# Kernel tuning notes

Measured on AMD Instinct MI355X. Metric: run time of the kernel, lower is better.

The kernel has to match this reference:

```python
import jax, jax.numpy as jnp
import numpy as np

NUM_GROUPS = 6
K = 40
CODEBOOK = 1024
VQ_COMMIT = 0.25


def setup_inputs() -> dict:
    key = jax.random.key(0)
    k1, k2 = jax.random.split(key)
    z = jax.random.normal(k1, (32, 60, 8000), dtype=jnp.float32)
    embeddings = jax.random.normal(k2, (NUM_GROUPS, K, CODEBOOK), dtype=jnp.float32)
    return {"z": z, "embeddings": embeddings}


def reference(z, embeddings):
    # z: (N, 60, T) -> reshape to (N, 240, T//4) as in Group_Quantize.forward
    N, C, T = z.shape
    z2 = z.reshape(N, C * 4, -1)          # (N, 240, Tp)
    Tp = z2.shape[-1]
    # split into groups and move channel last (EMAQuantizer transposes 1,-1)
    x = z2.reshape(N, NUM_GROUPS, K, Tp)
    x = jnp.transpose(x, (1, 0, 3, 2))    # (G, N, Tp, K)
    flat = x.reshape(NUM_GROUPS, N * Tp, K)  # (G, R, K)

    dist = (jnp.sum(flat ** 2, axis=-1, keepdims=True)
            - 2.0 * jnp.einsum('grk,gkc->grc', flat, embeddings)
            + jnp.sum(embeddings ** 2, axis=1)[:, None, :])  # (G, R, C)
    idx = jnp.argmin(dist, axis=-1)       # (G, R)

    # codebook lookup per group (embedding stored as (K, C), code vectors are columns)
    quant = jax.vmap(lambda e, i: jnp.take(e.T, i, axis=0))(embeddings, idx)  # (G, R, K)

    x4 = x                                 # (G, N, Tp, K)
    q4 = quant.reshape(NUM_GROUPS, N, Tp, K)

    # commitment loss per group, per batch element
    diff = VQ_COMMIT * jnp.mean((jax.lax.stop_gradient(q4) - x4) ** 2, axis=(2, 3))  # (G, N)
    vq_loss = jnp.sum(diff, axis=0) / NUM_GROUPS  # (N,)

    # straight-through estimator
    q_ste = x4 + jax.lax.stop_gradient(q4 - x4)   # (G, N, Tp, K)
    q_merge = jnp.transpose(q_ste, (1, 0, 3, 2)).reshape(N, NUM_GROUPS * K, Tp)  # (N, 240, Tp)
    q_merge = q_merge.reshape(N, (NUM_GROUPS * K) // 4, -1)  # (N, 60, T)
    return q_merge, vq_loss
```

## Files before the change

kernel.cpp:

```cpp
#include <hip/hip_runtime.h>
#include <math.h>

#define NG 6
#define KD 40
#define CB 1024
#define NB 32
#define TP 2000
#define RPB 128
#define THREADS 256
#define NBLK 500
#define ZN 480000
#define ZG 80000
#define BAND_D 6e-3f
#define PK_G 98304
#define PK_T 3072
#define CHS 6144
#define NCH 16

typedef __attribute__((ext_vector_type(8))) short bf16x8;
typedef __attribute__((ext_vector_type(16))) float f32x16;

__device__ __forceinline__ unsigned short bf16rne(float v) {
  unsigned u = __float_as_uint(v);
  return (unsigned short)((u + 0x7FFFu + ((u >> 16) & 1u)) >> 16);
}
__device__ __forceinline__ float bf16val(unsigned short h) {
  return __uint_as_float(((unsigned)h) << 16);
}
__device__ __forceinline__ void bf16split(float v, unsigned short& h, unsigned short& l) {
  h = bf16rne(v);
  l = bf16rne(v - bf16val(h));
}
__device__ __forceinline__ bf16x8 ldfrag16(const unsigned short* p) {
  union { uint4 q; bf16x8 v; } u;
  u.q = *(const uint4*)p;
  return u.v;
}
__device__ __forceinline__ void gload_lds16(const void* g, void* l) {
  __builtin_amdgcn_global_load_lds(
      (const __attribute__((address_space(1))) unsigned int*)g,
      (__attribute__((address_space(3))) unsigned int*)l, 16, 0, 0);
}

__global__ void prep_kernel(const float* __restrict__ emb, float* __restrict__ et,
                            float* __restrict__ e2, unsigned short* __restrict__ epack) {
  int c = blockIdx.x * blockDim.x + threadIdx.x;
  int g = blockIdx.y;
  if (c >= CB) return;
  const float* eg = emb + (size_t)g * KD * CB;
  float ev[KD];
  float* o = et + ((size_t)g * CB + c) * KD;
  float s = 0.f;
#pragma unroll
  for (int k = 0; k < KD; ++k) {
    float v = eg[k * CB + c];
    ev[k] = v;
    o[k] = v;
    s = __fadd_rn(s, __fmul_rn(v, v));
  }
  e2[g * CB + c] = s;

  float sv = 0.5f * s;
  unsigned short p0 = bf16rne(sv);
  float v1 = sv - bf16val(p0);
  unsigned short p1 = bf16rne(v1);
  unsigned short p2 = bf16rne(v1 - bf16val(p1));

  int tile = c >> 5, j32 = c & 31;
  unsigned short* tb = epack + (size_t)g * PK_G + (size_t)tile * PK_T;
#pragma unroll
  for (int s2 = 0; s2 < 3; ++s2)
#pragma unroll
    for (int gg = 0; gg < 2; ++gg) {
      union { uint4 q; unsigned short sh[8]; } uh, ul;
#pragma unroll
      for (int j = 0; j < 8; ++j) {
        int k = s2 * 16 + gg * 8 + j;
        if (k < KD) {
          bf16split(ev[k], uh.sh[j], ul.sh[j]);
        } else {
          uh.sh[j] = (k == 40) ? p0 : (k == 41) ? p1 : (k == 42) ? p2 : (unsigned short)0;
          ul.sh[j] = 0;
        }
      }
      unsigned short* ph = tb + ((size_t)(s2 * 2 + gg) * 32 + j32) * 8;
      *(uint4*)ph = uh.q;
      *(uint4*)(ph + 1536) = ul.q;
    }
}

__device__ __forceinline__ float npd_calc(const float* __restrict__ x,
                                          const float* __restrict__ ef,
                                          float e2c, float x2np) {
  float dot = 0.f;
#pragma unroll
  for (int k = 0; k < KD; ++k) dot = __fadd_rn(dot, __fmul_rn(x[k], ef[k]));
  return __fadd_rn(__fsub_rn(x2np, __fadd_rn(dot, dot)), e2c);
}

__global__ __launch_bounds__(THREADS, 4) void vq_kernel(
    const float* __restrict__ z, const float* __restrict__ et,
    const float* __restrict__ e2, const unsigned short* __restrict__ epack,
    float* __restrict__ out, float* __restrict__ partials) {
  const int g = blockIdx.y;
  const int bb = blockIdx.x;
  const int tid = threadIdx.x;
  const int lane = tid & 63;
  const int gg = lane >> 5;
  const int j32 = lane & 31;
  const int wid = tid >> 6;
  const int rowloc = wid * 32 + j32;
  const int rid = bb * RPB + rowloc;
  const int n = rid / TP;
  const int tt = rid - n * TP;

  const float* etg = et + (size_t)g * CB * KD;
  const float* e2g = e2 + g * CB;
  const unsigned short* egrp = epack + (size_t)g * PK_G;

  __shared__ __align__(16) unsigned short sbuf[2][CHS];
  __shared__ float r0s[THREADS], r1s[THREADS];

#define STAGE(B, CH) { \
    const unsigned short* gsrc = egrp + (size_t)(CH) * CHS + wid * 512 + lane * 8; \
    unsigned short* lb = &sbuf[B][wid * 512]; \
    gload_lds16(gsrc, lb); \
    gload_lds16(gsrc + 2048, lb + 2048); \
    gload_lds16(gsrc + 4096, lb + 4096); }
  STAGE(0, 0)

  const float* zp = z + (size_t)n * ZN + (size_t)g * ZG + tt;
  float x[KD];
#pragma unroll
  for (int k = 0; k < KD; ++k) x[k] = zp[(size_t)k * TP];
  float x2np;
  {
    float r[8];
#pragma unroll
    for (int j = 0; j < 8; ++j) r[j] = __fmul_rn(x[j], x[j]);
#pragma unroll
    for (int i = 8; i < KD; i += 8)
#pragma unroll
      for (int j = 0; j < 8; ++j)
        r[j] = __fadd_rn(r[j], __fmul_rn(x[i + j], x[i + j]));
    x2np = __fadd_rn(__fadd_rn(__fadd_rn(r[0], r[1]), __fadd_rn(r[2], r[3])),
                     __fadd_rn(__fadd_rn(r[4], r[5]), __fadd_rn(r[6], r[7])));
  }

  bf16x8 xh[3], xl[3];
#define PACK8(DH, DL, B0) { \
    union { unsigned short s[8]; bf16x8 v; } uh, ul; \
    _Pragma("unroll") \
    for (int j = 0; j < 8; ++j) { \
      unsigned short h, l; bf16split(-x[(B0) + j], h, l); \
      uh.s[j] = h; ul.s[j] = l; } \
    DH = uh.v; DL = ul.v; }
  if (gg == 0) {
    PACK8(xh[0], xl[0], 0)
    PACK8(xh[1], xl[1], 16)
    PACK8(xh[2], xl[2], 32)
  } else {
    PACK8(xh[0], xl[0], 8)
    PACK8(xh[1], xl[1], 24)
    union { unsigned short s[8]; bf16x8 v; } uh;
#pragma unroll
    for (int j = 0; j < 8; ++j) uh.s[j] = (j < 3) ? (unsigned short)0x3F80 : (unsigned short)0;
    xh[2] = uh.v;
    union { unsigned short s[8]; bf16x8 v; } uz;
#pragma unroll
    for (int j = 0; j < 8; ++j) uz.s[j] = 0;
    xl[2] = uz.v;
  }
#undef PACK8

  f32x16 zacc;
#pragma unroll
  for (int i = 0; i < 16; ++i) zacc[i] = 0.f;

  float d1 = INFINITY, d2x = INFINITY;
  int grp1 = 0;

#define TRACKG(AV, TILE) { \
    int cb = (TILE) * 32 + 4 * gg; \
    float g0 = fminf(fminf(fminf(AV[0], AV[1]), AV[2]), AV[3]); \
    float g1 = fminf(fminf(fminf(AV[4], AV[5]), AV[6]), AV[7]); \
    float g2 = fminf(fminf(fminf(AV[8], AV[9]), AV[10]), AV[11]); \
    float g3 = fminf(fminf(fminf(AV[12], AV[13]), AV[14]), AV[15]); \
    d2x = fminf(d2x, fmaxf(d1, g0)); grp1 = (g0 < d1) ? (cb + 0) : grp1; d1 = fminf(d1, g0); \
    d2x = fminf(d2x, fmaxf(d1, g1)); grp1 = (g1 < d1) ? (cb + 8) : grp1; d1 = fminf(d1, g1); \
    d2x = fminf(d2x, fmaxf(d1, g2)); grp1 = (g2 < d1) ? (cb + 16) : grp1; d1 = fminf(d1, g2); \
    d2x = fminf(d2x, fmaxf(d1, g3)); grp1 = (g3 < d1) ? (cb + 24) : grp1; d1 = fminf(d1, g3); }

#define MFMA9(TB, AOUT) { \
    bf16x8 eh0 = ldfrag16(TB); \
    bf16x8 eh1 = ldfrag16((TB) + 512); \
    bf16x8 eh2 = ldfrag16((TB) + 1024); \
    bf16x8 el0 = ldfrag16((TB) + 1536); \
    bf16x8 el1 = ldfrag16((TB) + 2048); \
    bf16x8 el2 = ldfrag16((TB) + 2560); \
    AOUT = __builtin_amdgcn_mfma_f32_32x32x16_bf16(eh0, xh[0], zacc, 0, 0, 0); \
    AOUT = __builtin_amdgcn_mfma_f32_32x32x16_bf16(eh0, xl[0], AOUT, 0, 0, 0); \
    AOUT = __builtin_amdgcn_mfma_f32_32x32x16_bf16(el0, xh[0], AOUT, 0, 0, 0); \
    AOUT = __builtin_amdgcn_mfma_f32_32x32x16_bf16(eh1, xh[1], AOUT, 0, 0, 0); \
    AOUT = __builtin_amdgcn_mfma_f32_32x32x16_bf16(eh1, xl[1], AOUT, 0, 0, 0); \
    AOUT = __builtin_amdgcn_mfma_f32_32x32x16_bf16(el1, xh[1], AOUT, 0, 0, 0); \
    AOUT = __builtin_amdgcn_mfma_f32_32x32x16_bf16(eh2, xh[2], AOUT, 0, 0, 0); \
    AOUT = __builtin_amdgcn_mfma_f32_32x32x16_bf16(eh2, xl[2], AOUT, 0, 0, 0); \
    AOUT = __builtin_amdgcn_mfma_f32_32x32x16_bf16(el2, xh[2], AOUT, 0, 0, 0); }

  int cur = 0;
#pragma unroll 1
  for (int ch = 0; ch < NCH; ++ch) {
    if (ch + 1 < NCH) {
      STAGE(cur ^ 1, ch + 1)
      asm volatile("s_waitcnt vmcnt(3)" ::: "memory");
    } else {
      asm volatile("s_waitcnt vmcnt(0)" ::: "memory");
    }
    __builtin_amdgcn_s_barrier();
    {
      const unsigned short* tb0 = &sbuf[cur][lane * 8];
      f32x16 a0;
      MFMA9(tb0, a0)
      TRACKG(a0, ch * 2)
      const unsigned short* tb1 = &sbuf[cur][PK_T + lane * 8];
      f32x16 a1;
      MFMA9(tb1, a1)
      TRACKG(a1, ch * 2 + 1)
    }
    __builtin_amdgcn_s_barrier();
    cur ^= 1;
  }

  float bd = INFINITY;
  int bi = CB;
#pragma unroll
  for (int j = 0; j < 4; ++j) {
    int c = grp1 + j;
    float d = npd_calc(x, etg + (size_t)c * KD, e2g[c], x2np);
    if (d < bd) { bd = d; bi = c; }
  }
  float dd2x = fmaf(2.f, d2x, x2np);

  {
    float od = __shfl_xor(bd, 32);
    int oi = __shfl_xor(bi, 32);
    float odd2x = __shfl_xor(dd2x, 32);
    if (od < bd || (od == bd && oi < bi)) { bd = od; bi = oi; }
    dd2x = fminf(dd2x, odd2x);
  }
  bool flag = dd2x < bd + BAND_D;

  if (__any(flag)) {
    float rd1 = INFINITY, rd2 = INFINITY, rd3 = INFINITY;
    int ri1 = 0, ri2 = 0, ri3 = 0;
#define INS3(V, C) { \
      bool u1 = (V) < rd1, u2 = (V) < rd2, u3 = (V) < rd3; \
      rd3 = u2 ? rd2 : (u3 ? (V) : rd3); ri3 = u2 ? ri2 : (u3 ? (C) : ri3); \
      rd2 = u1 ? rd1 : (u2 ? (V) : rd2); ri2 = u1 ? ri1 : (u2 ? (C) : ri2); \
      rd1 = u1 ? (V) : rd1;              ri1 = u1 ? (C) : ri1; }
#pragma unroll 1
    for (int tile = 0; tile < 32; ++tile) {
      const unsigned short* tb = egrp + (size_t)tile * PK_T + lane * 8;
      f32x16 a;
      MFMA9(tb, a)
      {
        float gm0 = fminf(fminf(a[0], a[1]), fminf(a[2], a[3]));
        float gm1 = fminf(fminf(a[4], a[5]), fminf(a[6], a[7]));
        float gm2 = fminf(fminf(a[8], a[9]), fminf(a[10], a[11]));
        float gm3 = fminf(fminf(a[12], a[13]), fminf(a[14], a[15]));
        float tmin = fminf(fminf(gm0, gm1), fminf(gm2, gm3));
        if (tmin < rd3) {
          int cb = tile * 32 + 4 * gg;
          if (gm0 < rd3) { INS3(a[0], cb + 0) INS3(a[1], cb + 1) INS3(a[2], cb + 2) INS3(a[3], cb + 3) }
          if (gm1 < rd3) { INS3(a[4], cb + 8) INS3(a[5], cb + 9) INS3(a[6], cb + 10) INS3(a[7], cb + 11) }
          if (gm2 < rd3) { INS3(a[8], cb + 16) INS3(a[9], cb + 17) INS3(a[10], cb + 18) INS3(a[11], cb + 19) }
          if (gm3 < rd3) { INS3(a[12], cb + 24) INS3(a[13], cb + 25) INS3(a[14], cb + 26) INS3(a[15], cb + 27) }
        }
      }
    }
    float dd1 = fmaf(2.f, rd1, x2np);
    float dd2 = fmaf(2.f, rd2, x2np);
    float dd3 = fmaf(2.f, rd3, x2np);
    bd = dd1; bi = ri1;
    bool exact = false;
    {
      bool need2 = dd2 < dd1 + BAND_D;
      bool need3 = dd3 < dd1 + BAND_D;
      if (need2 || need3) {
        int cA = ri1;
        int cB = need2 ? ri2 : 0x7fffffff;
        int cC = need3 ? ri3 : 0x7fffffff;
        int t;
        if (cA > cB) { t = cA; cA = cB; cB = t; }
        if (cB > cC) { t = cB; cB = cC; cC = t; }
        if (cA > cB) { t = cA; cA = cB; cB = t; }
        bd = INFINITY; bi = CB;
        if (cA < CB) { float d = npd_calc(x, etg + (size_t)cA * KD, e2g[cA], x2np); if (d < bd) { bd = d; bi = cA; } }
        if (cB < CB) { float d = npd_calc(x, etg + (size_t)cB * KD, e2g[cB], x2np); if (d < bd) { bd = d; bi = cB; } }
        if (cC < CB) { float d = npd_calc(x, etg + (size_t)cC * KD, e2g[cC], x2np); if (d < bd) { bd = d; bi = cC; } }
        exact = true;
      }
    }
    {
      float od = __shfl_xor(bd, 32);
      bool race = fabsf(bd - od) < BAND_D;
      if (race && !exact) bd = npd_calc(x, etg + (size_t)bi * KD, e2g[bi], x2np);
      float od2 = __shfl_xor(bd, 32);
      int oi = __shfl_xor(bi, 32);
      if (od2 < bd || (od2 == bd && oi < bi)) { bd = od2; bi = oi; }
    }
  }

  const float4* eb4 = (const float4*)(etg + (size_t)bi * KD);
  float* op = out + (size_t)n * ZN + (size_t)g * ZG + tt;
  float ls = 0.f;
  if (gg == 0) {
#pragma unroll
    for (int p = 0; p < 5; ++p) {
      float4 v = eb4[p];
      int k = 4 * p;
      float e0 = __fsub_rn(v.x, x[k + 0]); ls = fmaf(e0, e0, ls); op[(size_t)(k + 0) * TP] = __fadd_rn(x[k + 0], e0);
      float e1 = __fsub_rn(v.y, x[k + 1]); ls = fmaf(e1, e1, ls); op[(size_t)(k + 1) * TP] = __fadd_rn(x[k + 1], e1);
      float e2v = __fsub_rn(v.z, x[k + 2]); ls = fmaf(e2v, e2v, ls); op[(size_t)(k + 2) * TP] = __fadd_rn(x[k + 2], e2v);
      float e3 = __fsub_rn(v.w, x[k + 3]); ls = fmaf(e3, e3, ls); op[(size_t)(k + 3) * TP] = __fadd_rn(x[k + 3], e3);
    }
  } else {
#pragma unroll
    for (int p = 5; p < 10; ++p) {
      float4 v = eb4[p];
      int k = 4 * p;
      float e0 = __fsub_rn(v.x, x[k + 0]); ls = fmaf(e0, e0, ls); op[(size_t)(k + 0) * TP] = __fadd_rn(x[k + 0], e0);
      float e1 = __fsub_rn(v.y, x[k + 1]); ls = fmaf(e1, e1, ls); op[(size_t)(k + 1) * TP] = __fadd_rn(x[k + 1], e1);
      float e2v = __fsub_rn(v.z, x[k + 2]); ls = fmaf(e2v, e2v, ls); op[(size_t)(k + 2) * TP] = __fadd_rn(x[k + 2], e2v);
      float e3 = __fsub_rn(v.w, x[k + 3]); ls = fmaf(e3, e3, ls); op[(size_t)(k + 3) * TP] = __fadd_rn(x[k + 3], e3);
    }
  }

  const int n_lo = (bb * RPB) / TP;
  r0s[tid] = (n == n_lo) ? ls : 0.f;
  r1s[tid] = (n == n_lo) ? 0.f : ls;
  __syncthreads();
  for (int s = THREADS / 2; s > 0; s >>= 1) {
    if (tid < s) {
      r0s[tid] += r0s[tid + s];
      r1s[tid] += r1s[tid + s];
    }
    __syncthreads();
  }
  if (tid == 0) {
    partials[((size_t)g * NBLK + bb) * 2 + 0] = r0s[0];
    partials[((size_t)g * NBLK + bb) * 2 + 1] = r1s[0];
  }
}

__global__ void loss_kernel(const float* __restrict__ partials,
                            float* __restrict__ vq) {
  int n = threadIdx.x;
  if (n >= NB) return;
  float acc = 0.f;
  for (int g = 0; g < NG; ++g) {
    float s = 0.f;
    int b0 = (n * TP) / RPB;
    int b1 = ((n + 1) * TP - 1) / RPB;
    for (int b = b0; b <= b1; ++b) {
      int n_lo = (b * RPB) / TP;
      s += partials[((size_t)g * NBLK + b) * 2 + ((n == n_lo) ? 0 : 1)];
    }
    acc += 0.25f * (s / 80000.0f);
  }
  vq[n] = acc / 6.0f;
}

extern "C" void kernel_launch(void* const* d_in, const int* in_sizes, int n_in,
                              void* d_out, int out_size, void* d_ws, size_t ws_size,
                              hipStream_t stream) {
  const float* z = (const float*)d_in[0];
  const float* emb = (const float*)d_in[1];
  float* out = (float*)d_out;

  float* et = (float*)d_ws;
  float* e2 = et + (size_t)NG * CB * KD;
  float* partials = e2 + (size_t)NG * CB;
  unsigned short* epack = (unsigned short*)((char*)d_ws + 1031680);

  prep_kernel<<<dim3(CB / 256, NG), 256, 0, stream>>>(emb, et, e2, epack);
  vq_kernel<<<dim3(NBLK, NG), THREADS, 0, stream>>>(z, et, e2, epack, out, partials);
  loss_kernel<<<1, 64, 0, stream>>>(partials, out + (size_t)NB * 60 * 8000);
}
```

Measured before the change: 205.6 us.

## Switch codebook to single fp16 with split-x and widen rescore band

```diff
diff --git a/kernel.cpp b/kernel.cpp
--- a/kernel.cpp
+++ b/kernel.cpp
@@ -11,28 +11,27 @@
 #define NBLK 500
 #define ZN 480000
 #define ZG 80000
-#define BAND_D 6e-3f
-#define PK_G 98304
-#define PK_T 3072
+#define BAND_D 6e-2f
+#define PKH_G 49152
+#define PKH_T 1536
 #define CHS 6144
-#define NCH 16
-
-typedef __attribute__((ext_vector_type(8))) short bf16x8;
+#define NCH 8
+
+typedef __attribute__((ext_vector_type(8))) _Float16 f16x8;
 typedef __attribute__((ext_vector_type(16))) float f32x16;
 
-__device__ __forceinline__ unsigned short bf16rne(float v) {
-  unsigned u = __float_as_uint(v);
-  return (unsigned short)((u + 0x7FFFu + ((u >> 16) & 1u)) >> 16);
-}
-__device__ __forceinline__ float bf16val(unsigned short h) {
-  return __uint_as_float(((unsigned)h) << 16);
-}
-__device__ __forceinline__ void bf16split(float v, unsigned short& h, unsigned short& l) {
-  h = bf16rne(v);
-  l = bf16rne(v - bf16val(h));
-}
-__device__ __forceinline__ bf16x8 ldfrag16(const unsigned short* p) {
-  union { uint4 q; bf16x8 v; } u;
+__device__ __forceinline__ unsigned short f16h(float v) {
+  union { _Float16 h; unsigned short s; } u;
+  u.h = (_Float16)v;
+  return u.s;
+}
+__device__ __forceinline__ float f16f(unsigned short s) {
+  union { _Float16 h; unsigned short s; } u;
+  u.s = s;
+  return (float)u.h;
+}
+__device__ __forceinline__ f16x8 ldfragh(const unsigned short* p) {
+  union { uint4 q; f16x8 v; } u;
   u.q = *(const uint4*)p;
   return u.v;
 }
@@ -43,7 +42,7 @@
 }
 
 __global__ void prep_kernel(const float* __restrict__ emb, float* __restrict__ et,
-                            float* __restrict__ e2, unsigned short* __restrict__ epack) {
+                            float* __restrict__ e2, unsigned short* __restrict__ epackh) {
   int c = blockIdx.x * blockDim.x + threadIdx.x;
   int g = blockIdx.y;
   if (c >= CB) return;
@@ -61,31 +60,23 @@
   e2[g * CB + c] = s;
 
   float sv = 0.5f * s;
-  unsigned short p0 = bf16rne(sv);
-  float v1 = sv - bf16val(p0);
-  unsigned short p1 = bf16rne(v1);
-  unsigned short p2 = bf16rne(v1 - bf16val(p1));
+  unsigned short p0 = f16h(sv);
+  unsigned short p1 = f16h(sv - f16f(p0));
 
   int tile = c >> 5, j32 = c & 31;
-  unsigned short* tb = epack + (size_t)g * PK_G + (size_t)tile * PK_T;
+  unsigned short* tb = epackh + (size_t)g * PKH_G + (size_t)tile * PKH_T;
 #pragma unroll
   for (int s2 = 0; s2 < 3; ++s2)
 #pragma unroll
     for (int gg = 0; gg < 2; ++gg) {
-      union { uint4 q; unsigned short sh[8]; } uh, ul;
+      union { uint4 q; unsigned short sh[8]; } uh;
 #pragma unroll
       for (int j = 0; j < 8; ++j) {
         int k = s2 * 16 + gg * 8 + j;
-        if (k < KD) {
-          bf16split(ev[k], uh.sh[j], ul.sh[j]);
-        } else {
-          uh.sh[j] = (k == 40) ? p0 : (k == 41) ? p1 : (k == 42) ? p2 : (unsigned short)0;
-          ul.sh[j] = 0;
-        }
+        if (k < KD) uh.sh[j] = f16h(ev[k]);
+        else uh.sh[j] = (k == 40) ? p0 : (k == 41) ? p1 : (unsigned short)0;
       }
-      unsigned short* ph = tb + ((size_t)(s2 * 2 + gg) * 32 + j32) * 8;
-      *(uint4*)ph = uh.q;
-      *(uint4*)(ph + 1536) = ul.q;
+      *(uint4*)(tb + ((size_t)(s2 * 2 + gg) * 32 + j32) * 8) = uh.q;
     }
 }
 
@@ -98,9 +89,9 @@
   return __fadd_rn(__fsub_rn(x2np, __fadd_rn(dot, dot)), e2c);
 }
 
-__global__ __launch_bounds__(THREADS, 4) void vq_kernel(
+__global__ __launch_bounds__(THREADS, 3) void vq_kernel(
     const float* __restrict__ z, const float* __restrict__ et,
-    const float* __restrict__ e2, const unsigned short* __restrict__ epack,
+    const float* __restrict__ e2, const unsigned short* __restrict__ epackh,
     float* __restrict__ out, float* __restrict__ partials) {
   const int g = blockIdx.y;
   const int bb = blockIdx.x;
@@ -116,7 +107,7 @@
 
   const float* etg = et + (size_t)g * CB * KD;
   const float* e2g = e2 + g * CB;
-  const unsigned short* egrp = epack + (size_t)g * PK_G;
+  const unsigned short* egrp = epackh + (size_t)g * PKH_G;
 
   __shared__ __align__(16) unsigned short sbuf[2][CHS];
   __shared__ float r0s[THREADS], r1s[THREADS];
@@ -147,31 +138,32 @@
                      __fadd_rn(__fadd_rn(r[4], r[5]), __fadd_rn(r[6], r[7])));
   }
 
-  bf16x8 xh[3], xl[3];
-#define PACK8(DH, DL, B0) { \
-    union { unsigned short s[8]; bf16x8 v; } uh, ul; \
+  f16x8 xh[3], xl[3];
+#define PACKF(DH, DL, B0) { \
+    union { unsigned short s[8]; f16x8 v; } uh, ul; \
     _Pragma("unroll") \
     for (int j = 0; j < 8; ++j) { \
-      unsigned short h, l; bf16split(-x[(B0) + j], h, l); \
-      uh.s[j] = h; ul.s[j] = l; } \
+      float y = -x[(B0) + j]; \
+      unsigned short h = f16h(y); \
+      uh.s[j] = h; ul.s[j] = f16h(y - f16f(h)); } \
     DH = uh.v; DL = ul.v; }
   if (gg == 0) {
-    PACK8(xh[0], xl[0], 0)
-    PACK8(xh[1], xl[1], 16)
-    PACK8(xh[2], xl[2], 32)
+    PACKF(xh[0], xl[0], 0)
+    PACKF(xh[1], xl[1], 16)
+    PACKF(xh[2], xl[2], 32)
   } else {
-    PACK8(xh[0], xl[0], 8)
-    PACK8(xh[1], xl[1], 24)
-    union { unsigned short s[8]; bf16x8 v; } uh;
-#pragma unroll
-    for (int j = 0; j < 8; ++j) uh.s[j] = (j < 3) ? (unsigned short)0x3F80 : (unsigned short)0;
-    xh[2] = uh.v;
-    union { unsigned short s[8]; bf16x8 v; } uz;
-#pragma unroll
-    for (int j = 0; j < 8; ++j) uz.s[j] = 0;
+    PACKF(xh[0], xl[0], 8)
+    PACKF(xh[1], xl[1], 24)
+    union { unsigned short s[8]; f16x8 v; } uo, uz;
+#pragma unroll
+    for (int j = 0; j < 8; ++j) {
+      uo.s[j] = (j < 2) ? (unsigned short)0x3C00 : (unsigned short)0;
+      uz.s[j] = 0;
+    }
+    xh[2] = uo.v;
     xl[2] = uz.v;
   }
-#undef PACK8
+#undef PACKF
 
   f32x16 zacc;
 #pragma unroll
@@ -182,31 +174,25 @@
 
 #define TRACKG(AV, TILE) { \
     int cb = (TILE) * 32 + 4 * gg; \
-    float g0 = fminf(fminf(fminf(AV[0], AV[1]), AV[2]), AV[3]); \
-    float g1 = fminf(fminf(fminf(AV[4], AV[5]), AV[6]), AV[7]); \
-    float g2 = fminf(fminf(fminf(AV[8], AV[9]), AV[10]), AV[11]); \
-    float g3 = fminf(fminf(fminf(AV[12], AV[13]), AV[14]), AV[15]); \
-    d2x = fminf(d2x, fmaxf(d1, g0)); grp1 = (g0 < d1) ? (cb + 0) : grp1; d1 = fminf(d1, g0); \
-    d2x = fminf(d2x, fmaxf(d1, g1)); grp1 = (g1 < d1) ? (cb + 8) : grp1; d1 = fminf(d1, g1); \
-    d2x = fminf(d2x, fmaxf(d1, g2)); grp1 = (g2 < d1) ? (cb + 16) : grp1; d1 = fminf(d1, g2); \
-    d2x = fminf(d2x, fmaxf(d1, g3)); grp1 = (g3 < d1) ? (cb + 24) : grp1; d1 = fminf(d1, g3); }
-
-#define MFMA9(TB, AOUT) { \
-    bf16x8 eh0 = ldfrag16(TB); \
-    bf16x8 eh1 = ldfrag16((TB) + 512); \
-    bf16x8 eh2 = ldfrag16((TB) + 1024); \
-    bf16x8 el0 = ldfrag16((TB) + 1536); \
-    bf16x8 el1 = ldfrag16((TB) + 2048); \
-    bf16x8 el2 = ldfrag16((TB) + 2560); \
-    AOUT = __builtin_amdgcn_mfma_f32_32x32x16_bf16(eh0, xh[0], zacc, 0, 0, 0); \
-    AOUT = __builtin_amdgcn_mfma_f32_32x32x16_bf16(eh0, xl[0], AOUT, 0, 0, 0); \
-    AOUT = __builtin_amdgcn_mfma_f32_32x32x16_bf16(el0, xh[0], AOUT, 0, 0, 0); \
-    AOUT = __builtin_amdgcn_mfma_f32_32x32x16_bf16(eh1, xh[1], AOUT, 0, 0, 0); \
-    AOUT = __builtin_amdgcn_mfma_f32_32x32x16_bf16(eh1, xl[1], AOUT, 0, 0, 0); \
-    AOUT = __builtin_amdgcn_mfma_f32_32x32x16_bf16(el1, xh[1], AOUT, 0, 0, 0); \
-    AOUT = __builtin_amdgcn_mfma_f32_32x32x16_bf16(eh2, xh[2], AOUT, 0, 0, 0); \
-    AOUT = __builtin_amdgcn_mfma_f32_32x32x16_bf16(eh2, xl[2], AOUT, 0, 0, 0); \
-    AOUT = __builtin_amdgcn_mfma_f32_32x32x16_bf16(el2, xh[2], AOUT, 0, 0, 0); }
+    float q0 = fminf(fminf(fminf(AV[0], AV[1]), AV[2]), AV[3]); \
+    float q1 = fminf(fminf(fminf(AV[4], AV[5]), AV[6]), AV[7]); \
+    float q2 = fminf(fminf(fminf(AV[8], AV[9]), AV[10]), AV[11]); \
+    float q3 = fminf(fminf(fminf(AV[12], AV[13]), AV[14]), AV[15]); \
+    d2x = fminf(d2x, fmaxf(d1, q0)); grp1 = (q0 < d1) ? (cb + 0) : grp1; d1 = fminf(d1, q0); \
+    d2x = fminf(d2x, fmaxf(d1, q1)); grp1 = (q1 < d1) ? (cb + 8) : grp1; d1 = fminf(d1, q1); \
+    d2x = fminf(d2x, fmaxf(d1, q2)); grp1 = (q2 < d1) ? (cb + 16) : grp1; d1 = fminf(d1, q2); \
+    d2x = fminf(d2x, fmaxf(d1, q3)); grp1 = (q3 < d1) ? (cb + 24) : grp1; d1 = fminf(d1, q3); }
+
+#define MFMA6(TB, AOUT) { \
+    f16x8 e0 = ldfragh(TB); \
+    f16x8 e1 = ldfragh((TB) + 512); \
+    f16x8 e2f = ldfragh((TB) + 1024); \
+    AOUT = __builtin_amdgcn_mfma_f32_32x32x16_f16(e0, xh[0], zacc, 0, 0, 0); \
+    AOUT = __builtin_amdgcn_mfma_f32_32x32x16_f16(e0, xl[0], AOUT, 0, 0, 0); \
+    AOUT = __builtin_amdgcn_mfma_f32_32x32x16_f16(e1, xh[1], AOUT, 0, 0, 0); \
+    AOUT = __builtin_amdgcn_mfma_f32_32x32x16_f16(e1, xl[1], AOUT, 0, 0, 0); \
+    AOUT = __builtin_amdgcn_mfma_f32_32x32x16_f16(e2f, xh[2], AOUT, 0, 0, 0); \
+    AOUT = __builtin_amdgcn_mfma_f32_32x32x16_f16(e2f, xl[2], AOUT, 0, 0, 0); }
 
   int cur = 0;
 #pragma unroll 1
@@ -219,14 +205,15 @@
     }
     __builtin_amdgcn_s_barrier();
     {
-      const unsigned short* tb0 = &sbuf[cur][lane * 8];
-      f32x16 a0;
-      MFMA9(tb0, a0)
-      TRACKG(a0, ch * 2)
-      const unsigned short* tb1 = &sbuf[cur][PK_T + lane * 8];
-      f32x16 a1;
-      MFMA9(tb1, a1)
-      TRACKG(a1, ch * 2 + 1)
+      f32x16 a0, a1, a2, a3;
+      MFMA6(&sbuf[cur][0 * PKH_T + lane * 8], a0)
+      MFMA6(&sbuf[cur][1 * PKH_T + lane * 8], a1)
+      MFMA6(&sbuf[cur][2 * PKH_T + lane * 8], a2)
+      MFMA6(&sbuf[cur][3 * PKH_T + lane * 8], a3)
+      TRACKG(a0, ch * 4 + 0)
+      TRACKG(a1, ch * 4 + 1)
+      TRACKG(a2, ch * 4 + 2)
+      TRACKG(a3, ch * 4 + 3)
     }
     __builtin_amdgcn_s_barrier();
     cur ^= 1;
@@ -261,9 +248,9 @@
       rd1 = u1 ? (V) : rd1;              ri1 = u1 ? (C) : ri1; }
 #pragma unroll 1
     for (int tile = 0; tile < 32; ++tile) {
-      const unsigned short* tb = egrp + (size_t)tile * PK_T + lane * 8;
+      const unsigned short* tb = egrp + (size_t)tile * PKH_T + lane * 8;
       f32x16 a;
-      MFMA9(tb, a)
+      MFMA6(tb, a)
       {
         float gm0 = fminf(fminf(a[0], a[1]), fminf(a[2], a[3]));
         float gm1 = fminf(fminf(a[4], a[5]), fminf(a[6], a[7]));
@@ -382,9 +369,9 @@
   float* et = (float*)d_ws;
   float* e2 = et + (size_t)NG * CB * KD;
   float* partials = e2 + (size_t)NG * CB;
-  unsigned short* epack = (unsigned short*)((char*)d_ws + 1031680);
-
-  prep_kernel<<<dim3(CB / 256, NG), 256, 0, stream>>>(emb, et, e2, epack);
-  vq_kernel<<<dim3(NBLK, NG), THREADS, 0, stream>>>(z, et, e2, epack, out, partials);
+  unsigned short* epackh = (unsigned short*)((char*)d_ws + 1031680);
+
+  prep_kernel<<<dim3(CB / 256, NG), 256, 0, stream>>>(emb, et, e2, epackh);
+  vq_kernel<<<dim3(NBLK, NG), THREADS, 0, stream>>>(z, et, e2, epackh, out, partials);
   loss_kernel<<<1, 64, 0, stream>>>(partials, out + (size_t)NB * 60 * 8000);
 }
```

Measured after the change: 260.2 us. +26.6%, slower.

## Track top-two candidate groups to shrink exact-rescan fallback frequency

Applied to the files above, without the earlier changes.

```diff
diff --git a/kernel.cpp b/kernel.cpp
--- a/kernel.cpp
+++ b/kernel.cpp
@@ -98,7 +98,7 @@
   return __fadd_rn(__fsub_rn(x2np, __fadd_rn(dot, dot)), e2c);
 }
 
-__global__ __launch_bounds__(THREADS, 4) void vq_kernel(
+__global__ __launch_bounds__(THREADS, 3) void vq_kernel(
     const float* __restrict__ z, const float* __restrict__ et,
     const float* __restrict__ e2, const unsigned short* __restrict__ epack,
     float* __restrict__ out, float* __restrict__ partials) {
@@ -177,19 +177,35 @@
 #pragma unroll
   for (int i = 0; i < 16; ++i) zacc[i] = 0.f;
 
-  float d1 = INFINITY, d2x = INFINITY;
-  int grp1 = 0;
+  float d1 = INFINITY, d2x = INFINITY, d3x = INFINITY;
+  int grp1 = 0, grp2 = 0;
 
 #define TRACKG(AV, TILE) { \
     int cb = (TILE) * 32 + 4 * gg; \
-    float g0 = fminf(fminf(fminf(AV[0], AV[1]), AV[2]), AV[3]); \
-    float g1 = fminf(fminf(fminf(AV[4], AV[5]), AV[6]), AV[7]); \
-    float g2 = fminf(fminf(fminf(AV[8], AV[9]), AV[10]), AV[11]); \
-    float g3 = fminf(fminf(fminf(AV[12], AV[13]), AV[14]), AV[15]); \
-    d2x = fminf(d2x, fmaxf(d1, g0)); grp1 = (g0 < d1) ? (cb + 0) : grp1; d1 = fminf(d1, g0); \
-    d2x = fminf(d2x, fmaxf(d1, g1)); grp1 = (g1 < d1) ? (cb + 8) : grp1; d1 = fminf(d1, g1); \
-    d2x = fminf(d2x, fmaxf(d1, g2)); grp1 = (g2 < d1) ? (cb + 16) : grp1; d1 = fminf(d1, g2); \
-    d2x = fminf(d2x, fmaxf(d1, g3)); grp1 = (g3 < d1) ? (cb + 24) : grp1; d1 = fminf(d1, g3); }
+    float q0 = fminf(fminf(fminf(AV[0], AV[1]), AV[2]), AV[3]); \
+    float q1 = fminf(fminf(fminf(AV[4], AV[5]), AV[6]), AV[7]); \
+    float q2 = fminf(fminf(fminf(AV[8], AV[9]), AV[10]), AV[11]); \
+    float q3 = fminf(fminf(fminf(AV[12], AV[13]), AV[14]), AV[15]); \
+    { bool b1 = q0 < d1, b2 = q0 < d2x; \
+      d3x = fminf(d3x, fmaxf(d2x, q0)); \
+      grp2 = b1 ? grp1 : (b2 ? (cb + 0) : grp2); \
+      d2x = fminf(d2x, fmaxf(d1, q0)); \
+      grp1 = b1 ? (cb + 0) : grp1; d1 = fminf(d1, q0); } \
+    { bool b1 = q1 < d1, b2 = q1 < d2x; \
+      d3x = fminf(d3x, fmaxf(d2x, q1)); \
+      grp2 = b1 ? grp1 : (b2 ? (cb + 8) : grp2); \
+      d2x = fminf(d2x, fmaxf(d1, q1)); \
+      grp1 = b1 ? (cb + 8) : grp1; d1 = fminf(d1, q1); } \
+    { bool b1 = q2 < d1, b2 = q2 < d2x; \
+      d3x = fminf(d3x, fmaxf(d2x, q2)); \
+      grp2 = b1 ? grp1 : (b2 ? (cb + 16) : grp2); \
+      d2x = fminf(d2x, fmaxf(d1, q2)); \
+      grp1 = b1 ? (cb + 16) : grp1; d1 = fminf(d1, q2); } \
+    { bool b1 = q3 < d1, b2 = q3 < d2x; \
+      d3x = fminf(d3x, fmaxf(d2x, q3)); \
+      grp2 = b1 ? grp1 : (b2 ? (cb + 24) : grp2); \
+      d2x = fminf(d2x, fmaxf(d1, q3)); \
+      grp1 = b1 ? (cb + 24) : grp1; d1 = fminf(d1, q3); } }
 
 #define MFMA9(TB, AOUT) { \
     bf16x8 eh0 = ldfrag16(TB); \
@@ -219,13 +235,10 @@
     }
     __builtin_amdgcn_s_barrier();
     {
-      const unsigned short* tb0 = &sbuf[cur][lane * 8];
-      f32x16 a0;
-      MFMA9(tb0, a0)
+      f32x16 a0, a1;
+      MFMA9(&sbuf[cur][lane * 8], a0)
+      MFMA9(&sbuf[cur][PK_T + lane * 8], a1)
       TRACKG(a0, ch * 2)
-      const unsigned short* tb1 = &sbuf[cur][PK_T + lane * 8];
-      f32x16 a1;
-      MFMA9(tb1, a1)
       TRACKG(a1, ch * 2 + 1)
     }
     __builtin_amdgcn_s_barrier();
@@ -234,22 +247,29 @@
 
   float bd = INFINITY;
   int bi = CB;
+#define UPD(DV, CV) { if ((DV) < bd || ((DV) == bd && (CV) < bi)) { bd = (DV); bi = (CV); } }
 #pragma unroll
   for (int j = 0; j < 4; ++j) {
     int c = grp1 + j;
     float d = npd_calc(x, etg + (size_t)c * KD, e2g[c], x2np);
-    if (d < bd) { bd = d; bi = c; }
-  }
-  float dd2x = fmaf(2.f, d2x, x2np);
+    UPD(d, c)
+  }
+#pragma unroll
+  for (int j = 0; j < 4; ++j) {
+    int c = grp2 + j;
+    float d = npd_calc(x, etg + (size_t)c * KD, e2g[c], x2np);
+    UPD(d, c)
+  }
+  float dd3x = fmaf(2.f, d3x, x2np);
 
   {
     float od = __shfl_xor(bd, 32);
     int oi = __shfl_xor(bi, 32);
-    float odd2x = __shfl_xor(dd2x, 32);
+    float odd3x = __shfl_xor(dd3x, 32);
     if (od < bd || (od == bd && oi < bi)) { bd = od; bi = oi; }
-    dd2x = fminf(dd2x, odd2x);
-  }
-  bool flag = dd2x < bd + BAND_D;
+    dd3x = fminf(dd3x, odd3x);
+  }
+  bool flag = dd3x < bd + BAND_D;
 
   if (__any(flag)) {
     float rd1 = INFINITY, rd2 = INFINITY, rd3 = INFINITY;
```

Result: slower. 228.7 us (+11.2%).

## Triple-buffer codebook chunks in LDS and drop the trailing barrier

Applied to the files above, without the earlier changes.

```diff
diff --git a/kernel.cpp b/kernel.cpp
--- a/kernel.cpp
+++ b/kernel.cpp
@@ -98,7 +98,7 @@
   return __fadd_rn(__fsub_rn(x2np, __fadd_rn(dot, dot)), e2c);
 }
 
-__global__ __launch_bounds__(THREADS, 4) void vq_kernel(
+__global__ __launch_bounds__(THREADS, 3) void vq_kernel(
     const float* __restrict__ z, const float* __restrict__ et,
     const float* __restrict__ e2, const unsigned short* __restrict__ epack,
     float* __restrict__ out, float* __restrict__ partials) {
@@ -118,7 +118,7 @@
   const float* e2g = e2 + g * CB;
   const unsigned short* egrp = epack + (size_t)g * PK_G;
 
-  __shared__ __align__(16) unsigned short sbuf[2][CHS];
+  __shared__ __align__(16) unsigned short sbuf[3][CHS];
   __shared__ float r0s[THREADS], r1s[THREADS];
 
 #define STAGE(B, CH) { \
@@ -128,6 +128,7 @@
     gload_lds16(gsrc + 2048, lb + 2048); \
     gload_lds16(gsrc + 4096, lb + 4096); }
   STAGE(0, 0)
+  STAGE(1, 1)
 
   const float* zp = z + (size_t)n * ZN + (size_t)g * ZG + tt;
   float x[KD];
@@ -182,14 +183,14 @@
 
 #define TRACKG(AV, TILE) { \
     int cb = (TILE) * 32 + 4 * gg; \
-    float g0 = fminf(fminf(fminf(AV[0], AV[1]), AV[2]), AV[3]); \
-    float g1 = fminf(fminf(fminf(AV[4], AV[5]), AV[6]), AV[7]); \
-    float g2 = fminf(fminf(fminf(AV[8], AV[9]), AV[10]), AV[11]); \
-    float g3 = fminf(fminf(fminf(AV[12], AV[13]), AV[14]), AV[15]); \
-    d2x = fminf(d2x, fmaxf(d1, g0)); grp1 = (g0 < d1) ? (cb + 0) : grp1; d1 = fminf(d1, g0); \
-    d2x = fminf(d2x, fmaxf(d1, g1)); grp1 = (g1 < d1) ? (cb + 8) : grp1; d1 = fminf(d1, g1); \
-    d2x = fminf(d2x, fmaxf(d1, g2)); grp1 = (g2 < d1) ? (cb + 16) : grp1; d1 = fminf(d1, g2); \
-    d2x = fminf(d2x, fmaxf(d1, g3)); grp1 = (g3 < d1) ? (cb + 24) : grp1; d1 = fminf(d1, g3); }
+    float q0 = fminf(fminf(fminf(AV[0], AV[1]), AV[2]), AV[3]); \
+    float q1 = fminf(fminf(fminf(AV[4], AV[5]), AV[6]), AV[7]); \
+    float q2 = fminf(fminf(fminf(AV[8], AV[9]), AV[10]), AV[11]); \
+    float q3 = fminf(fminf(fminf(AV[12], AV[13]), AV[14]), AV[15]); \
+    d2x = fminf(d2x, fmaxf(d1, q0)); grp1 = (q0 < d1) ? (cb + 0) : grp1; d1 = fminf(d1, q0); \
+    d2x = fminf(d2x, fmaxf(d1, q1)); grp1 = (q1 < d1) ? (cb + 8) : grp1; d1 = fminf(d1, q1); \
+    d2x = fminf(d2x, fmaxf(d1, q2)); grp1 = (q2 < d1) ? (cb + 16) : grp1; d1 = fminf(d1, q2); \
+    d2x = fminf(d2x, fmaxf(d1, q3)); grp1 = (q3 < d1) ? (cb + 24) : grp1; d1 = fminf(d1, q3); }
 
 #define MFMA9(TB, AOUT) { \
     bf16x8 eh0 = ldfrag16(TB); \
@@ -208,28 +209,25 @@
     AOUT = __builtin_amdgcn_mfma_f32_32x32x16_bf16(eh2, xl[2], AOUT, 0, 0, 0); \
     AOUT = __builtin_amdgcn_mfma_f32_32x32x16_bf16(el2, xh[2], AOUT, 0, 0, 0); }
 
-  int cur = 0;
+  int cur = 0, stg = 2;
 #pragma unroll 1
   for (int ch = 0; ch < NCH; ++ch) {
-    if (ch + 1 < NCH) {
-      STAGE(cur ^ 1, ch + 1)
+    if (ch < NCH - 1) {
       asm volatile("s_waitcnt vmcnt(3)" ::: "memory");
     } else {
       asm volatile("s_waitcnt vmcnt(0)" ::: "memory");
     }
     __builtin_amdgcn_s_barrier();
+    if (ch + 2 < NCH) STAGE(stg, ch + 2)
     {
-      const unsigned short* tb0 = &sbuf[cur][lane * 8];
-      f32x16 a0;
-      MFMA9(tb0, a0)
+      f32x16 a0, a1;
+      MFMA9(&sbuf[cur][lane * 8], a0)
+      MFMA9(&sbuf[cur][PK_T + lane * 8], a1)
       TRACKG(a0, ch * 2)
-      const unsigned short* tb1 = &sbuf[cur][PK_T + lane * 8];
-      f32x16 a1;
-      MFMA9(tb1, a1)
       TRACKG(a1, ch * 2 + 1)
     }
-    __builtin_amdgcn_s_barrier();
-    cur ^= 1;
+    cur = (cur == 2) ? 0 : cur + 1;
+    stg = (stg == 2) ? 0 : stg + 1;
   }
 
   float bd = INFINITY;
```

New measurement: 205.9 us. Within noise of the previous version (+0.2%).
